# Kernel tuning notes

Hardware: AMD Instinct MI355X
Metric: run time of the kernel (lower is better)

Reference implementation:

```python
import jax, jax.numpy as jnp
import numpy as np

B = 65536   # batch (agent-timesteps)
NN = 16     # neighbors per agent
NO = 32     # obstacles per agent
SD = 4      # state_dim_per_agent
D_ROBOT = 0.3
D_OBST = 0.5
B_GAMMA = 0.01
B_EXPH = 1.0
A_MIN, A_MAX = -2.0, 2.0
PHI_MIN, PHI_MAX = -2.0, 2.0


def _mlp2(h, W1, b1, W2, b2):
    # DeepSet sub-network: activation between layers, linear last (matches
    # 'for layer in layers[:-1]: x = act(layer(x)); x = layers[-1](x)')
    return jax.nn.relu(h @ W1 + b1) @ W2 + b2


def setup_inputs() -> dict:
    key = jax.random.key(0)
    ks = jax.random.split(key, 24)
    own = jax.random.normal(ks[0], (B, SD), dtype=jnp.float32)
    # relative positions with |component| in [0.5, 2.0] so norms exceed D_* (barrier well-defined)
    npos = jax.random.uniform(ks[1], (B, NN, 2), minval=0.5, maxval=2.0) * jnp.sign(jax.random.normal(ks[2], (B, NN, 2)))
    nvel = 0.1 * jax.random.normal(ks[3], (B, NN, 2))
    neigh = jnp.concatenate([npos, nvel], axis=-1).reshape(B, 4 * NN)
    opos = (jax.random.uniform(ks[4], (B, NO, 2), minval=0.5, maxval=2.0) * jnp.sign(jax.random.normal(ks[5], (B, NO, 2)))).reshape(B, 2 * NO)
    x = jnp.concatenate([jnp.full((B, 1), float(NN), dtype=jnp.float32), own, neigh, opos], axis=1)
    noise = 0.05 * jax.random.normal(ks[6], (B, 2), dtype=jnp.float32)  # the 0.05*N(0,1) action noise, made deterministic

    def lin(k, i, o):
        return 0.1 * jax.random.normal(k, (i, o), dtype=jnp.float32)

    return {
        'x': x, 'noise': noise,
        # neighbor DeepSet: phi 4->64->16, rho 16->64->8
        'pnW1': lin(ks[7], 4, 64),  'pnb1': jnp.zeros((64,), jnp.float32),
        'pnW2': lin(ks[8], 64, 16), 'pnb2': jnp.zeros((16,), jnp.float32),
        'rnW1': lin(ks[9], 16, 64), 'rnb1': jnp.zeros((64,), jnp.float32),
        'rnW2': lin(ks[10], 64, 8), 'rnb2': jnp.zeros((8,), jnp.float32),
        # obstacle DeepSet: phi 2->64->16, rho 16->64->8
        'poW1': lin(ks[11], 2, 64),  'pob1': jnp.zeros((64,), jnp.float32),
        'poW2': lin(ks[12], 64, 16), 'pob2': jnp.zeros((16,), jnp.float32),
        'roW1': lin(ks[13], 16, 64), 'rob1': jnp.zeros((64,), jnp.float32),
        'roW2': lin(ks[14], 64, 8),  'rob2': jnp.zeros((8,), jnp.float32),
        # psi: 18 -> 64 -> 64 -> 2
        'psW1': lin(ks[15], 18, 64), 'psb1': jnp.zeros((64,), jnp.float32),
        'psW2': lin(ks[16], 64, 64), 'psb2': jnp.zeros((64,), jnp.float32),
        'psW3': lin(ks[17], 64, 2),  'psb3': jnp.zeros((2,), jnp.float32),
    }


def reference(x, noise,
              pnW1, pnb1, pnW2, pnb2, rnW1, rnb1, rnW2, rnb2,
              poW1, pob1, poW2, pob2, roW1, rob1, roW2, rob2,
              psW1, psb1, psW2, psb2, psW3, psb3):
    b = x.shape[0]
    neigh = x[:, 5:5 + 4 * NN].reshape(b, NN, 4)   # per-neighbor relative state
    obst = x[:, 5 + 4 * NN:].reshape(b, NO, 2)      # per-obstacle relative pos

    # 'empty' (learned) action: DeepSets + psi MLP
    rho_n = _mlp2(_mlp2(neigh, pnW1, pnb1, pnW2, pnb2).sum(axis=1), rnW1, rnb1, rnW2, rnb2)
    rho_o = _mlp2(_mlp2(obst, poW1, pob1, poW2, pob2).sum(axis=1), roW1, rob1, roW2, rob2)
    g = x[:, 1:3]
    h = jnp.concatenate([rho_n, rho_o, g], axis=1)
    h = jax.nn.relu(h @ psW1 + psb1)
    h = jax.nn.relu(h @ psW2 + psb2)
    h = jnp.tanh(h @ psW3 + psb3)
    empty = (h + 1.0) / 2.0 * (PHI_MAX - PHI_MIN) + PHI_MIN

    # barrier terms, vectorized over all neighbors/obstacles at once:
    # A = b_gamma * P * ||P||^-1 * (||P|| - D)^(-b_exph), summed over edges
    def barrier_sum(P, D):
        nrm = jnp.linalg.norm(P, axis=-1, keepdims=True)   # [b, E, 1]
        H = nrm - D
        return (B_GAMMA * P / (nrm * H ** B_EXPH)).sum(axis=1)

    bar = barrier_sum(-neigh[..., :2], D_ROBOT) + barrier_sum(-obst, D_OBST)

    a = jnp.tanh(empty + bar + noise)
    return (a + 1.0) / 2.0 * (A_MAX - A_MIN) + A_MIN
```

## Files before the change

kernel.cpp:

```cpp
#include <hip/hip_runtime.h>

#define NN 16
#define NO 32
#define XCOLS 133

typedef _Float16 h8v __attribute__((ext_vector_type(8)));
typedef _Float16 h2 __attribute__((ext_vector_type(2)));
typedef float f4v __attribute__((ext_vector_type(4)));
typedef unsigned ui4 __attribute__((ext_vector_type(4)));
typedef float f2u __attribute__((ext_vector_type(2), aligned(4)));

static __device__ __forceinline__ f4v MFMA(h8v a, h8v b, f4v c) {
    return __builtin_amdgcn_mfma_f32_16x16x32_f16(a, b, c, 0, 0, 0);
}
static __device__ __forceinline__ unsigned pkbits(float a, float b) {
    return __builtin_bit_cast(unsigned, __builtin_amdgcn_cvt_pkrtz(a, b));
}
static __device__ __forceinline__ h2 u2h(unsigned v) { return __builtin_bit_cast(h2, v); }

__global__ void prep_frags(
    const float* __restrict__ pnW1, const float* __restrict__ pnW2,
    const float* __restrict__ rnW1, const float* __restrict__ rnW2,
    const float* __restrict__ poW1, const float* __restrict__ poW2,
    const float* __restrict__ roW1, const float* __restrict__ roW2,
    const float* __restrict__ psW1, const float* __restrict__ psW2,
    const float* __restrict__ psW3, unsigned* __restrict__ ws)
{
    const float* Ws[11] = {pnW1,pnW2,rnW1,rnW2,poW1,poW2,roW1,roW2,psW1,psW2,psW3};
    const int Kr[11]   = {4,64,16,64,2,64,16,64,18,64,64};
    const int Nr[11]   = {64,16,64,8,64,16,64,8,64,64,2};
    const int nkc[11]  = {1,2,1,2,1,2,1,2,1,2,2};
    const int nnt[11]  = {4,1,4,1,4,1,4,1,4,4,1};
    const int base[11] = {0,1024,1536,2560,3072,4096,4608,5632,6144,7168,9216};

    const int gid = blockIdx.x * 256 + threadIdx.x;
    int start = 0;
    #pragma unroll
    for (int a2 = 0; a2 < 11; ++a2) {
        const int n = nkc[a2] * nnt[a2] * 256;
        if (gid >= start && gid < start + n) {
            const int i = gid - start;
            const float* Wm = Ws[a2];
            const int K = Kr[a2], N = Nr[a2], nt_n = nnt[a2];
            const int d = i & 3, lane = (i >> 2) & 63, t = i >> 8;
            const int nt = t % nt_n, kc = t / nt_n;
            const int k = kc * 32 + 8 * (lane >> 4) + 2 * d;
            const int col = nt * 16 + (lane & 15);
            const float v0 = (k     < K && col < N) ? Wm[(k    ) * N + col] : 0.f;
            const float v1 = (k + 1 < K && col < N) ? Wm[(k + 1) * N + col] : 0.f;
            ws[base[a2] + i] = pkbits(v0, v1);
        }
        start += n;
    }
}

__global__ __launch_bounds__(64, 4) void barrier_net_kernel(
    const float* __restrict__ x, const float* __restrict__ noise,
    const float* __restrict__ pnb1, const float* __restrict__ pnb2,
    const float* __restrict__ rnb1, const float* __restrict__ rnb2,
    const float* __restrict__ pob1, const float* __restrict__ pob2,
    const float* __restrict__ rob1, const float* __restrict__ rob2,
    const float* __restrict__ psb1, const float* __restrict__ psb2,
    const float* __restrict__ psb3,
    const unsigned* __restrict__ wsu, float* __restrict__ out)
{
    __shared__ unsigned XS[16 * 66];
    __shared__ _Float16 W[3136];

    const int l = threadIdx.x;
    const int r = l & 15;
    const int g = l >> 4;
    const int eb = blockIdx.x * 16;

    float* barf = (float*)(W + 3072);
    const h8v* FB = (const h8v*)wsu;

    {
        const float* base = x + (size_t)eb * XCOLS;
        f2u raw[16];
        #pragma unroll
        for (int it = 0; it < 16; ++it)
            raw[it] = *(const f2u*)(base + (size_t)it * XCOLS + 5 + 2 * l);
        f2u graw = {0.f, 0.f};
        if (l < 16) graw = *(const f2u*)(base + (size_t)l * XCOLS + 1);
        #pragma unroll
        for (int it = 0; it < 16; ++it)
            XS[it * 66 + l] = pkbits(raw[it][0], raw[it][1]);
        if (l < 16) XS[l * 66 + 64] = pkbits(graw[0], graw[1]);
    }

    {
        unsigned* z = (unsigned*)(W + 2048);
        #pragma unroll
        for (int i = 0; i < 8; ++i) z[l + 64 * i] = 0u;
    }

    const int rowb = r * 66;
    const int sw8 = (r & 7) << 3;
    const int sw4 = (r & 3) << 3;

    {
        float bq0 = 0.f, bq1 = 0.f;
        #pragma unroll
        for (int jj = 0; jj < 4; ++jj) {
            const h2 v = u2h(XS[rowb + 2 * (4 * g + jj)]);
            const float v0 = (float)v[0], v1 = (float)v[1];
            const float nrm = sqrtf(v0*v0 + v1*v1);
            const float cc = 0.01f * __builtin_amdgcn_rcpf(nrm * (nrm - 0.3f));
            bq0 -= cc * v0; bq1 -= cc * v1;
        }
        #pragma unroll
        for (int jj = 0; jj < 8; ++jj) {
            const h2 v = u2h(XS[rowb + 32 + 8 * g + jj]);
            const float v0 = (float)v[0], v1 = (float)v[1];
            const float nrm = sqrtf(v0*v0 + v1*v1);
            const float cc = 0.01f * __builtin_amdgcn_rcpf(nrm * (nrm - 0.5f));
            bq0 -= cc * v0; bq1 -= cc * v1;
        }
        bq0 += __shfl_xor(bq0, 16); bq0 += __shfl_xor(bq0, 32);
        bq1 += __shfl_xor(bq1, 16); bq1 += __shfl_xor(bq1, 32);
        if (g == 0) { barf[2*r] = bq0; barf[2*r + 1] = bq1; }
    }

    {
        const h8v B0 = FB[0*64 + l], B1 = FB[1*64 + l];
        const h8v B2 = FB[2*64 + l], B3 = FB[3*64 + l];
        const f4v c0 = {pnb1[r], pnb1[r], pnb1[r], pnb1[r]};
        const f4v c1 = {pnb1[16+r], pnb1[16+r], pnb1[16+r], pnb1[16+r]};
        const f4v c2 = {pnb1[32+r], pnb1[32+r], pnb1[32+r], pnb1[32+r]};
        const f4v c3 = {pnb1[48+r], pnb1[48+r], pnb1[48+r], pnb1[48+r]};
        f4v s0 = {0,0,0,0}, s1 = {0,0,0,0}, s2 = {0,0,0,0}, s3 = {0,0,0,0};
        #pragma unroll 4
        for (int j = 0; j < NN; ++j) {
            const uint2 np = *(const uint2*)&XS[rowb + 2 * j];
            ui4 au = {np.x, np.y, 0u, 0u};
            const h8v a = __builtin_bit_cast(h8v, au);
            const f4v d0 = MFMA(a, B0, c0);
            const f4v d1 = MFMA(a, B1, c1);
            const f4v d2 = MFMA(a, B2, c2);
            const f4v d3 = MFMA(a, B3, c3);
            #pragma unroll
            for (int q = 0; q < 4; ++q) {
                s0[q] += fmaxf(d0[q], 0.f); s1[q] += fmaxf(d1[q], 0.f);
                s2[q] += fmaxf(d2[q], 0.f); s3[q] += fmaxf(d3[q], 0.f);
            }
        }
        #pragma unroll
        for (int q = 0; q < 4; ++q) {
            const int e = 4 * g + q;
            const int m = (e & 7) << 3;
            W[e*64 + (( 0 + r) ^ m)] = (_Float16)s0[q];
            W[e*64 + ((16 + r) ^ m)] = (_Float16)s1[q];
            W[e*64 + ((32 + r) ^ m)] = (_Float16)s2[q];
            W[e*64 + ((48 + r) ^ m)] = (_Float16)s3[q];
        }
    }

    {
        const h8v B0 = FB[768 + 0*64 + l], B1 = FB[768 + 1*64 + l];
        const h8v B2 = FB[768 + 2*64 + l], B3 = FB[768 + 3*64 + l];
        const f4v c0 = {pob1[r], pob1[r], pob1[r], pob1[r]};
        const f4v c1 = {pob1[16+r], pob1[16+r], pob1[16+r], pob1[16+r]};
        const f4v c2 = {pob1[32+r], pob1[32+r], pob1[32+r], pob1[32+r]};
        const f4v c3 = {pob1[48+r], pob1[48+r], pob1[48+r], pob1[48+r]};
        f4v s0 = {0,0,0,0}, s1 = {0,0,0,0}, s2 = {0,0,0,0}, s3 = {0,0,0,0};
        #pragma unroll 2
        for (int t = 0; t < 16; ++t) {
            const uint2 op = *(const uint2*)&XS[rowb + 32 + 2 * t];
            ui4 au0 = {op.x, 0u, 0u, 0u};
            ui4 au1 = {op.y, 0u, 0u, 0u};
            const h8v a0 = __builtin_bit_cast(h8v, au0);
            const h8v a1 = __builtin_bit_cast(h8v, au1);
            const f4v d0 = MFMA(a0, B0, c0); const f4v e0 = MFMA(a1, B0, c0);
            const f4v d1 = MFMA(a0, B1, c1); const f4v e1 = MFMA(a1, B1, c1);
            const f4v d2 = MFMA(a0, B2, c2); const f4v e2 = MFMA(a1, B2, c2);
            const f4v d3 = MFMA(a0, B3, c3); const f4v e3 = MFMA(a1, B3, c3);
            #pragma unroll
            for (int q = 0; q < 4; ++q) {
                s0[q] += fmaxf(d0[q], 0.f) + fmaxf(e0[q], 0.f);
                s1[q] += fmaxf(d1[q], 0.f) + fmaxf(e1[q], 0.f);
                s2[q] += fmaxf(d2[q], 0.f) + fmaxf(e2[q], 0.f);
                s3[q] += fmaxf(d3[q], 0.f) + fmaxf(e3[q], 0.f);
            }
        }
        #pragma unroll
        for (int q = 0; q < 4; ++q) {
            const int e = 4 * g + q;
            const int m = (e & 7) << 3;
            W[1024 + e*64 + (( 0 + r) ^ m)] = (_Float16)s0[q];
            W[1024 + e*64 + ((16 + r) ^ m)] = (_Float16)s1[q];
            W[1024 + e*64 + ((32 + r) ^ m)] = (_Float16)s2[q];
            W[1024 + e*64 + ((48 + r) ^ m)] = (_Float16)s3[q];
        }
    }

    {
        h8v a0 = *(const h8v*)&W[r*64 + (( 0 + 8*g) ^ sw8)];
        h8v a1 = *(const h8v*)&W[r*64 + ((32 + 8*g) ^ sw8)];
        h8v b0 = FB[256 + 0*64 + l];
        h8v b1 = FB[256 + 1*64 + l];
        const float bb = 16.f * pnb2[r];
        f4v c = {bb, bb, bb, bb};
        f4v d = MFMA(a1, b1, MFMA(a0, b0, c));
        #pragma unroll
        for (int q = 0; q < 4; ++q) {
            const int row = 4 * g + q;
            W[2048 + row*32 + (r ^ ((row&3)<<3))] = (_Float16)d[q];
        }
    }
    {
        h8v a = *(const h8v*)&W[2048 + r*32 + ((8*g) ^ sw4)];
        #pragma unroll
        for (int nt = 0; nt < 4; ++nt) {
            h8v b = FB[384 + nt*64 + l];
            const float bb = rnb1[16*nt + r];
            f4v c = {bb, bb, bb, bb};
            f4v d = MFMA(a, b, c);
            #pragma unroll
            for (int q = 0; q < 4; ++q) {
                const int row = 4 * g + q;
                W[row*64 + ((16*nt + r) ^ ((row&7)<<3))] = (_Float16)fmaxf(d[q], 0.f);
            }
        }
    }
    {
        h8v a0 = *(const h8v*)&W[r*64 + (( 0 + 8*g) ^ sw8)];
        h8v a1 = *(const h8v*)&W[r*64 + ((32 + 8*g) ^ sw8)];
        h8v b0 = FB[640 + 0*64 + l];
        h8v b1 = FB[640 + 1*64 + l];
        const float bb = (r < 8) ? rnb2[r & 7] : 0.f;
        f4v c = {bb, bb, bb, bb};
        f4v d = MFMA(a1, b1, MFMA(a0, b0, c));
        if (r < 8) {
            #pragma unroll
            for (int q = 0; q < 4; ++q) {
                const int row = 4 * g + q;
                W[2560 + row*32 + (r ^ ((row&3)<<3))] = (_Float16)d[q];
            }
        }
    }
    {
        h8v a0 = *(const h8v*)&W[1024 + r*64 + (( 0 + 8*g) ^ sw8)];
        h8v a1 = *(const h8v*)&W[1024 + r*64 + ((32 + 8*g) ^ sw8)];
        h8v b0 = FB[1024 + 0*64 + l];
        h8v b1 = FB[1024 + 1*64 + l];
        const float bb = 32.f * pob2[r];
        f4v c = {bb, bb, bb, bb};
        f4v d = MFMA(a1, b1, MFMA(a0, b0, c));
        #pragma unroll
        for (int q = 0; q < 4; ++q) {
            const int row = 4 * g + q;
            W[2048 + row*32 + (r ^ ((row&3)<<3))] = (_Float16)d[q];
        }
    }
    {
        h8v a = *(const h8v*)&W[2048 + r*32 + ((8*g) ^ sw4)];
        #pragma unroll
        for (int nt = 0; nt < 4; ++nt) {
            h8v b = FB[1152 + nt*64 + l];
            const float bb = rob1[16*nt + r];
            f4v c = {bb, bb, bb, bb};
            f4v d = MFMA(a, b, c);
            #pragma unroll
            for (int q = 0; q < 4; ++q) {
                const int row = 4 * g + q;
                W[row*64 + ((16*nt + r) ^ ((row&7)<<3))] = (_Float16)fmaxf(d[q], 0.f);
            }
        }
    }
    {
        h8v a0 = *(const h8v*)&W[r*64 + (( 0 + 8*g) ^ sw8)];
        h8v a1 = *(const h8v*)&W[r*64 + ((32 + 8*g) ^ sw8)];
        h8v b0 = FB[1408 + 0*64 + l];
        h8v b1 = FB[1408 + 1*64 + l];
        const float bb = (r < 8) ? rob2[r & 7] : 0.f;
        f4v c = {bb, bb, bb, bb};
        f4v d = MFMA(a1, b1, MFMA(a0, b0, c));
        if (r < 8) {
            #pragma unroll
            for (int q = 0; q < 4; ++q) {
                const int row = 4 * g + q;
                W[2560 + row*32 + ((8 + r) ^ ((row&3)<<3))] = (_Float16)d[q];
            }
        }
    }
    if (g == 0) {
        const h2 gv = u2h(XS[rowb + 64]);
        W[2560 + r*32 + (16 ^ sw4)] = gv[0];
        W[2560 + r*32 + (17 ^ sw4)] = gv[1];
    }
    {
        h8v a = *(const h8v*)&W[2560 + r*32 + ((8*g) ^ sw4)];
        #pragma unroll
        for (int nt = 0; nt < 4; ++nt) {
            h8v b = FB[1536 + nt*64 + l];
            const float bb = psb1[16*nt + r];
            f4v c = {bb, bb, bb, bb};
            f4v d = MFMA(a, b, c);
            #pragma unroll
            for (int q = 0; q < 4; ++q) {
                const int row = 4 * g + q;
                W[1024 + row*64 + ((16*nt + r) ^ ((row&7)<<3))] = (_Float16)fmaxf(d[q], 0.f);
            }
        }
    }
    {
        h8v a0 = *(const h8v*)&W[1024 + r*64 + (( 0 + 8*g) ^ sw8)];
        h8v a1 = *(const h8v*)&W[1024 + r*64 + ((32 + 8*g) ^ sw8)];
        #pragma unroll
        for (int nt = 0; nt < 4; ++nt) {
            h8v b0 = FB[1792 + (0*4 + nt)*64 + l];
            h8v b1 = FB[1792 + (1*4 + nt)*64 + l];
            const float bb = psb2[16*nt + r];
            f4v c = {bb, bb, bb, bb};
            f4v d = MFMA(a1, b1, MFMA(a0, b0, c));
            #pragma unroll
            for (int q = 0; q < 4; ++q) {
                const int row = 4 * g + q;
                W[row*64 + ((16*nt + r) ^ ((row&7)<<3))] = (_Float16)fmaxf(d[q], 0.f);
            }
        }
    }
    f4v dOut;
    {
        h8v a0 = *(const h8v*)&W[r*64 + (( 0 + 8*g) ^ sw8)];
        h8v a1 = *(const h8v*)&W[r*64 + ((32 + 8*g) ^ sw8)];
        h8v b0 = FB[2304 + 0*64 + l];
        h8v b1 = FB[2304 + 1*64 + l];
        const float bb = (r < 2) ? psb3[r & 1] : 0.f;
        f4v c = {bb, bb, bb, bb};
        dOut = MFMA(a1, b1, MFMA(a0, b0, c));
    }
    if (r < 2) {
        #pragma unroll
        for (int q = 0; q < 4; ++q) {
            const int e = 4 * g + q;
            const float o = dOut[q];
            const float bar = barf[e*2 + r];
            const float nz = noise[2 * (size_t)(eb + e) + r];
            const float av = tanhf(2.f * tanhf(o) + bar + nz);
            out[2 * (size_t)(eb + e) + r] = 2.f * av;
        }
    }
}

extern "C" void kernel_launch(void* const* d_in, const int* in_sizes, int n_in,
                              void* d_out, int out_size, void* d_ws, size_t ws_size,
                              hipStream_t stream) {
    const float* x    = (const float*)d_in[0];
    const float* nz   = (const float*)d_in[1];
    const float* pnW1 = (const float*)d_in[2];
    const float* pnb1 = (const float*)d_in[3];
    const float* pnW2 = (const float*)d_in[4];
    const float* pnb2 = (const float*)d_in[5];
    const float* rnW1 = (const float*)d_in[6];
    const float* rnb1 = (const float*)d_in[7];
    const float* rnW2 = (const float*)d_in[8];
    const float* rnb2 = (const float*)d_in[9];
    const float* poW1 = (const float*)d_in[10];
    const float* pob1 = (const float*)d_in[11];
    const float* poW2 = (const float*)d_in[12];
    const float* pob2 = (const float*)d_in[13];
    const float* roW1 = (const float*)d_in[14];
    const float* rob1 = (const float*)d_in[15];
    const float* roW2 = (const float*)d_in[16];
    const float* rob2 = (const float*)d_in[17];
    const float* psW1 = (const float*)d_in[18];
    const float* psb1 = (const float*)d_in[19];
    const float* psW2 = (const float*)d_in[20];
    const float* psb2 = (const float*)d_in[21];
    const float* psW3 = (const float*)d_in[22];
    const float* psb3 = (const float*)d_in[23];

    unsigned* ws = (unsigned*)d_ws;
    hipLaunchKernelGGL(prep_frags, dim3(38), dim3(256), 0, stream,
        pnW1, pnW2, rnW1, rnW2, poW1, poW2, roW1, roW2, psW1, psW2, psW3, ws);

    const int b = in_sizes[0] / XCOLS;
    hipLaunchKernelGGL(barrier_net_kernel, dim3(b / 16), dim3(64), 0, stream,
        x, nz, pnb1, pnb2, rnb1, rnb2, pob1, pob2, rob1, rob2,
        psb1, psb2, psb3, ws, (float*)d_out);
}
```

Baseline: 44.68 us.

## Process two 16-row tiles per wavefront to reuse weight fragments

Each 64-thread block now handles 32 agents as two 16-row sub-tiles, with separate LDS scratch per sub-tile. Weight fragments and biases are loaded once and applied to both sub-tiles, and the independent MFMA chains are interleaved to hide latency. The goal is to cut repeated global weight loads and per-block overhead. In exchange the grid is halved, register and LDS use per wave roughly double, and launch bounds drop to 2 waves per SIMD, which may reduce occupancy.

```diff
diff --git a/kernel.cpp b/kernel.cpp
--- a/kernel.cpp
+++ b/kernel.cpp
@@ -54,7 +54,7 @@
     }
 }
 
-__global__ __launch_bounds__(64, 4) void barrier_net_kernel(
+__global__ __launch_bounds__(64, 2) void barrier_net_kernel(
     const float* __restrict__ x, const float* __restrict__ noise,
     const float* __restrict__ pnb1, const float* __restrict__ pnb2,
     const float* __restrict__ rnb1, const float* __restrict__ rnb2,
@@ -64,42 +64,50 @@
     const float* __restrict__ psb3,
     const unsigned* __restrict__ wsu, float* __restrict__ out)
 {
-    __shared__ unsigned XS[16 * 66];
-    __shared__ _Float16 W[3136];
+    __shared__ unsigned XS[32 * 66];
+    __shared__ _Float16 W[2 * 3136];
 
     const int l = threadIdx.x;
     const int r = l & 15;
     const int g = l >> 4;
-    const int eb = blockIdx.x * 16;
-
-    float* barf = (float*)(W + 3072);
+    const int eb = blockIdx.x * 32;
+
     const h8v* FB = (const h8v*)wsu;
-
-    {
-        const float* base = x + (size_t)eb * XCOLS;
-        f2u raw[16];
-        #pragma unroll
-        for (int it = 0; it < 16; ++it)
-            raw[it] = *(const f2u*)(base + (size_t)it * XCOLS + 5 + 2 * l);
-        f2u graw = {0.f, 0.f};
-        if (l < 16) graw = *(const f2u*)(base + (size_t)l * XCOLS + 1);
-        #pragma unroll
-        for (int it = 0; it < 16; ++it)
-            XS[it * 66 + l] = pkbits(raw[it][0], raw[it][1]);
-        if (l < 16) XS[l * 66 + 64] = pkbits(graw[0], graw[1]);
-    }
-
-    {
-        unsigned* z = (unsigned*)(W + 2048);
-        #pragma unroll
-        for (int i = 0; i < 8; ++i) z[l + 64 * i] = 0u;
-    }
-
-    const int rowb = r * 66;
     const int sw8 = (r & 7) << 3;
     const int sw4 = (r & 3) << 3;
 
     {
+        const float* base = x + (size_t)eb * XCOLS;
+        #pragma unroll
+        for (int half = 0; half < 2; ++half) {
+            f2u raw[16];
+            #pragma unroll
+            for (int it = 0; it < 16; ++it)
+                raw[it] = *(const f2u*)(base + (size_t)(16 * half + it) * XCOLS + 5 + 2 * l);
+            #pragma unroll
+            for (int it = 0; it < 16; ++it)
+                XS[(16 * half + it) * 66 + l] = pkbits(raw[it][0], raw[it][1]);
+        }
+        if (l < 32) {
+            const f2u graw = *(const f2u*)(base + (size_t)l * XCOLS + 1);
+            XS[l * 66 + 64] = pkbits(graw[0], graw[1]);
+        }
+    }
+
+    {
+        #pragma unroll
+        for (int s = 0; s < 2; ++s) {
+            unsigned* z = (unsigned*)(W + s * 3136 + 2048);
+            #pragma unroll
+            for (int i = 0; i < 8; ++i) z[l + 64 * i] = 0u;
+        }
+    }
+
+    #pragma unroll
+    for (int s = 0; s < 2; ++s) {
+        _Float16* Ws_ = W + s * 3136;
+        float* barf = (float*)(Ws_ + 3072);
+        const int rowb = (16 * s + r) * 66;
         float bq0 = 0.f, bq1 = 0.f;
         #pragma unroll
         for (int jj = 0; jj < 4; ++jj) {
@@ -119,8 +127,16 @@
         }
         bq0 += __shfl_xor(bq0, 16); bq0 += __shfl_xor(bq0, 32);
         bq1 += __shfl_xor(bq1, 16); bq1 += __shfl_xor(bq1, 32);
-        if (g == 0) { barf[2*r] = bq0; barf[2*r + 1] = bq1; }
-    }
+        if (g == 0) {
+            barf[2*r] = bq0; barf[2*r + 1] = bq1;
+            const h2 gv = u2h(XS[rowb + 64]);
+            Ws_[2560 + r*32 + (16 ^ sw4)] = gv[0];
+            Ws_[2560 + r*32 + (17 ^ sw4)] = gv[1];
+        }
+    }
+
+    const int rowbA = r * 66;
+    const int rowbB = (16 + r) * 66;
 
     {
         const h8v B0 = FB[0*64 + l], B1 = FB[1*64 + l];
@@ -129,30 +145,44 @@
         const f4v c1 = {pnb1[16+r], pnb1[16+r], pnb1[16+r], pnb1[16+r]};
         const f4v c2 = {pnb1[32+r], pnb1[32+r], pnb1[32+r], pnb1[32+r]};
         const f4v c3 = {pnb1[48+r], pnb1[48+r], pnb1[48+r], pnb1[48+r]};
-        f4v s0 = {0,0,0,0}, s1 = {0,0,0,0}, s2 = {0,0,0,0}, s3 = {0,0,0,0};
+        f4v sA0 = {0,0,0,0}, sA1 = {0,0,0,0}, sA2 = {0,0,0,0}, sA3 = {0,0,0,0};
+        f4v sB0 = {0,0,0,0}, sB1 = {0,0,0,0}, sB2 = {0,0,0,0}, sB3 = {0,0,0,0};
         #pragma unroll 4
         for (int j = 0; j < NN; ++j) {
-            const uint2 np = *(const uint2*)&XS[rowb + 2 * j];
-            ui4 au = {np.x, np.y, 0u, 0u};
-            const h8v a = __builtin_bit_cast(h8v, au);
-            const f4v d0 = MFMA(a, B0, c0);
-            const f4v d1 = MFMA(a, B1, c1);
-            const f4v d2 = MFMA(a, B2, c2);
-            const f4v d3 = MFMA(a, B3, c3);
+            const uint2 npA = *(const uint2*)&XS[rowbA + 2 * j];
+            const uint2 npB = *(const uint2*)&XS[rowbB + 2 * j];
+            ui4 auA = {npA.x, npA.y, 0u, 0u};
+            ui4 auB = {npB.x, npB.y, 0u, 0u};
+            const h8v aA = __builtin_bit_cast(h8v, auA);
+            const h8v aB = __builtin_bit_cast(h8v, auB);
+            const f4v dA0 = MFMA(aA, B0, c0);
+            const f4v dA1 = MFMA(aA, B1, c1);
+            const f4v dA2 = MFMA(aA, B2, c2);
+            const f4v dA3 = MFMA(aA, B3, c3);
+            const f4v dB0 = MFMA(aB, B0, c0);
+            const f4v dB1 = MFMA(aB, B1, c1);
+            const f4v dB2 = MFMA(aB, B2, c2);
+            const f4v dB3 = MFMA(aB, B3, c3);
             #pragma unroll
             for (int q = 0; q < 4; ++q) {
-                s0[q] += fmaxf(d0[q], 0.f); s1[q] += fmaxf(d1[q], 0.f);
-                s2[q] += fmaxf(d2[q], 0.f); s3[q] += fmaxf(d3[q], 0.f);
+                sA0[q] += fmaxf(dA0[q], 0.f); sA1[q] += fmaxf(dA1[q], 0.f);
+                sA2[q] += fmaxf(dA2[q], 0.f); sA3[q] += fmaxf(dA3[q], 0.f);
+                sB0[q] += fmaxf(dB0[q], 0.f); sB1[q] += fmaxf(dB1[q], 0.f);
+                sB2[q] += fmaxf(dB2[q], 0.f); sB3[q] += fmaxf(dB3[q], 0.f);
             }
         }
         #pragma unroll
         for (int q = 0; q < 4; ++q) {
             const int e = 4 * g + q;
             const int m = (e & 7) << 3;
-            W[e*64 + (( 0 + r) ^ m)] = (_Float16)s0[q];
-            W[e*64 + ((16 + r) ^ m)] = (_Float16)s1[q];
-            W[e*64 + ((32 + r) ^ m)] = (_Float16)s2[q];
-            W[e*64 + ((48 + r) ^ m)] = (_Float16)s3[q];
+            W[e*64 + (( 0 + r) ^ m)] = (_Float16)sA0[q];
+            W[e*64 + ((16 + r) ^ m)] = (_Float16)sA1[q];
+            W[e*64 + ((32 + r) ^ m)] = (_Float16)sA2[q];
+            W[e*64 + ((48 + r) ^ m)] = (_Float16)sA3[q];
+            W[3136 + e*64 + (( 0 + r) ^ m)] = (_Float16)sB0[q];
+            W[3136 + e*64 + ((16 + r) ^ m)] = (_Float16)sB1[q];
+            W[3136 + e*64 + ((32 + r) ^ m)] = (_Float16)sB2[q];
+            W[3136 + e*64 + ((48 + r) ^ m)] = (_Float16)sB3[q];
         }
     }
 
@@ -163,183 +193,230 @@
         const f4v c1 = {pob1[16+r], pob1[16+r], pob1[16+r], pob1[16+r]};
         const f4v c2 = {pob1[32+r], pob1[32+r], pob1[32+r], pob1[32+r]};
         const f4v c3 = {pob1[48+r], pob1[48+r], pob1[48+r], pob1[48+r]};
-        f4v s0 = {0,0,0,0}, s1 = {0,0,0,0}, s2 = {0,0,0,0}, s3 = {0,0,0,0};
+        f4v sA0 = {0,0,0,0}, sA1 = {0,0,0,0}, sA2 = {0,0,0,0}, sA3 = {0,0,0,0};
+        f4v sB0 = {0,0,0,0}, sB1 = {0,0,0,0}, sB2 = {0,0,0,0}, sB3 = {0,0,0,0};
         #pragma unroll 2
         for (int t = 0; t < 16; ++t) {
-            const uint2 op = *(const uint2*)&XS[rowb + 32 + 2 * t];
-            ui4 au0 = {op.x, 0u, 0u, 0u};
-            ui4 au1 = {op.y, 0u, 0u, 0u};
-            const h8v a0 = __builtin_bit_cast(h8v, au0);
-            const h8v a1 = __builtin_bit_cast(h8v, au1);
-            const f4v d0 = MFMA(a0, B0, c0); const f4v e0 = MFMA(a1, B0, c0);
-            const f4v d1 = MFMA(a0, B1, c1); const f4v e1 = MFMA(a1, B1, c1);
-            const f4v d2 = MFMA(a0, B2, c2); const f4v e2 = MFMA(a1, B2, c2);
-            const f4v d3 = MFMA(a0, B3, c3); const f4v e3 = MFMA(a1, B3, c3);
+            const uint2 opA = *(const uint2*)&XS[rowbA + 32 + 2 * t];
+            const uint2 opB = *(const uint2*)&XS[rowbB + 32 + 2 * t];
+            ui4 aA0u = {opA.x, 0u, 0u, 0u}; ui4 aA1u = {opA.y, 0u, 0u, 0u};
+            ui4 aB0u = {opB.x, 0u, 0u, 0u}; ui4 aB1u = {opB.y, 0u, 0u, 0u};
+            const h8v aA0 = __builtin_bit_cast(h8v, aA0u);
+            const h8v aA1 = __builtin_bit_cast(h8v, aA1u);
+            const h8v aB0 = __builtin_bit_cast(h8v, aB0u);
+            const h8v aB1 = __builtin_bit_cast(h8v, aB1u);
+            const f4v dA0 = MFMA(aA0, B0, c0); const f4v eA0 = MFMA(aA1, B0, c0);
+            const f4v dA1 = MFMA(aA0, B1, c1); const f4v eA1 = MFMA(aA1, B1, c1);
+            const f4v dA2 = MFMA(aA0, B2, c2); const f4v eA2 = MFMA(aA1, B2, c2);
+            const f4v dA3 = MFMA(aA0, B3, c3); const f4v eA3 = MFMA(aA1, B3, c3);
+            const f4v dB0 = MFMA(aB0, B0, c0); const f4v eB0 = MFMA(aB1, B0, c0);
+            const f4v dB1 = MFMA(aB0, B1, c1); const f4v eB1 = MFMA(aB1, B1, c1);
+            const f4v dB2 = MFMA(aB0, B2, c2); const f4v eB2 = MFMA(aB1, B2, c2);
+            const f4v dB3 = MFMA(aB0, B3, c3); const f4v eB3 = MFMA(aB1, B3, c3);
             #pragma unroll
             for (int q = 0; q < 4; ++q) {
-                s0[q] += fmaxf(d0[q], 0.f) + fmaxf(e0[q], 0.f);
-                s1[q] += fmaxf(d1[q], 0.f) + fmaxf(e1[q], 0.f);
-                s2[q] += fmaxf(d2[q], 0.f) + fmaxf(e2[q], 0.f);
-                s3[q] += fmaxf(d3[q], 0.f) + fmaxf(e3[q], 0.f);
+                sA0[q] += fmaxf(dA0[q], 0.f) + fmaxf(eA0[q], 0.f);
+                sA1[q] += fmaxf(dA1[q], 0.f) + fmaxf(eA1[q], 0.f);
+                sA2[q] += fmaxf(dA2[q], 0.f) + fmaxf(eA2[q], 0.f);
+                sA3[q] += fmaxf(dA3[q], 0.f) + fmaxf(eA3[q], 0.f);
+                sB0[q] += fmaxf(dB0[q], 0.f) + fmaxf(eB0[q], 0.f);
+                sB1[q] += fmaxf(dB1[q], 0.f) + fmaxf(eB1[q], 0.f);
+                sB2[q] += fmaxf(dB2[q], 0.f) + fmaxf(eB2[q], 0.f);
+                sB3[q] += fmaxf(dB3[q], 0.f) + fmaxf(eB3[q], 0.f);
             }
         }
         #pragma unroll
         for (int q = 0; q < 4; ++q) {
             const int e = 4 * g + q;
             const int m = (e & 7) << 3;
-            W[1024 + e*64 + (( 0 + r) ^ m)] = (_Float16)s0[q];
-            W[1024 + e*64 + ((16 + r) ^ m)] = (_Float16)s1[q];
-            W[1024 + e*64 + ((32 + r) ^ m)] = (_Float16)s2[q];
-            W[1024 + e*64 + ((48 + r) ^ m)] = (_Float16)s3[q];
-        }
-    }
-
-    {
-        h8v a0 = *(const h8v*)&W[r*64 + (( 0 + 8*g) ^ sw8)];
-        h8v a1 = *(const h8v*)&W[r*64 + ((32 + 8*g) ^ sw8)];
+            W[1024 + e*64 + (( 0 + r) ^ m)] = (_Float16)sA0[q];
+            W[1024 + e*64 + ((16 + r) ^ m)] = (_Float16)sA1[q];
+            W[1024 + e*64 + ((32 + r) ^ m)] = (_Float16)sA2[q];
+            W[1024 + e*64 + ((48 + r) ^ m)] = (_Float16)sA3[q];
+            W[3136 + 1024 + e*64 + (( 0 + r) ^ m)] = (_Float16)sB0[q];
+            W[3136 + 1024 + e*64 + ((16 + r) ^ m)] = (_Float16)sB1[q];
+            W[3136 + 1024 + e*64 + ((32 + r) ^ m)] = (_Float16)sB2[q];
+            W[3136 + 1024 + e*64 + ((48 + r) ^ m)] = (_Float16)sB3[q];
+        }
+    }
+
+    {
         h8v b0 = FB[256 + 0*64 + l];
         h8v b1 = FB[256 + 1*64 + l];
         const float bb = 16.f * pnb2[r];
-        f4v c = {bb, bb, bb, bb};
-        f4v d = MFMA(a1, b1, MFMA(a0, b0, c));
-        #pragma unroll
-        for (int q = 0; q < 4; ++q) {
-            const int row = 4 * g + q;
-            W[2048 + row*32 + (r ^ ((row&3)<<3))] = (_Float16)d[q];
-        }
-    }
-    {
-        h8v a = *(const h8v*)&W[2048 + r*32 + ((8*g) ^ sw4)];
+        const f4v c = {bb, bb, bb, bb};
+        #pragma unroll
+        for (int s = 0; s < 2; ++s) {
+            _Float16* Ws_ = W + s * 3136;
+            h8v a0 = *(const h8v*)&Ws_[r*64 + (( 0 + 8*g) ^ sw8)];
+            h8v a1 = *(const h8v*)&Ws_[r*64 + ((32 + 8*g) ^ sw8)];
+            f4v d = MFMA(a1, b1, MFMA(a0, b0, c));
+            #pragma unroll
+            for (int q = 0; q < 4; ++q) {
+                const int row = 4 * g + q;
+                Ws_[2048 + row*32 + (r ^ ((row&3)<<3))] = (_Float16)d[q];
+            }
+        }
+    }
+    {
         #pragma unroll
         for (int nt = 0; nt < 4; ++nt) {
             h8v b = FB[384 + nt*64 + l];
             const float bb = rnb1[16*nt + r];
-            f4v c = {bb, bb, bb, bb};
-            f4v d = MFMA(a, b, c);
-            #pragma unroll
-            for (int q = 0; q < 4; ++q) {
-                const int row = 4 * g + q;
-                W[row*64 + ((16*nt + r) ^ ((row&7)<<3))] = (_Float16)fmaxf(d[q], 0.f);
-            }
-        }
-    }
-    {
-        h8v a0 = *(const h8v*)&W[r*64 + (( 0 + 8*g) ^ sw8)];
-        h8v a1 = *(const h8v*)&W[r*64 + ((32 + 8*g) ^ sw8)];
+            const f4v c = {bb, bb, bb, bb};
+            #pragma unroll
+            for (int s = 0; s < 2; ++s) {
+                _Float16* Ws_ = W + s * 3136;
+                h8v a = *(const h8v*)&Ws_[2048 + r*32 + ((8*g) ^ sw4)];
+                f4v d = MFMA(a, b, c);
+                #pragma unroll
+                for (int q = 0; q < 4; ++q) {
+                    const int row = 4 * g + q;
+                    Ws_[row*64 + ((16*nt + r) ^ ((row&7)<<3))] = (_Float16)fmaxf(d[q], 0.f);
+                }
+            }
+        }
+    }
+    {
         h8v b0 = FB[640 + 0*64 + l];
         h8v b1 = FB[640 + 1*64 + l];
         const float bb = (r < 8) ? rnb2[r & 7] : 0.f;
-        f4v c = {bb, bb, bb, bb};
-        f4v d = MFMA(a1, b1, MFMA(a0, b0, c));
-        if (r < 8) {
-            #pragma unroll
-            for (int q = 0; q < 4; ++q) {
-                const int row = 4 * g + q;
-                W[2560 + row*32 + (r ^ ((row&3)<<3))] = (_Float16)d[q];
-            }
-        }
-    }
-    {
-        h8v a0 = *(const h8v*)&W[1024 + r*64 + (( 0 + 8*g) ^ sw8)];
-        h8v a1 = *(const h8v*)&W[1024 + r*64 + ((32 + 8*g) ^ sw8)];
+        const f4v c = {bb, bb, bb, bb};
+        #pragma unroll
+        for (int s = 0; s < 2; ++s) {
+            _Float16* Ws_ = W + s * 3136;
+            h8v a0 = *(const h8v*)&Ws_[r*64 + (( 0 + 8*g) ^ sw8)];
+            h8v a1 = *(const h8v*)&Ws_[r*64 + ((32 + 8*g) ^ sw8)];
+            f4v d = MFMA(a1, b1, MFMA(a0, b0, c));
+            if (r < 8) {
+                #pragma unroll
+                for (int q = 0; q < 4; ++q) {
+                    const int row = 4 * g + q;
+                    Ws_[2560 + row*32 + (r ^ ((row&3)<<3))] = (_Float16)d[q];
+                }
+            }
+        }
+    }
+    {
         h8v b0 = FB[1024 + 0*64 + l];
         h8v b1 = FB[1024 + 1*64 + l];
         const float bb = 32.f * pob2[r];
-        f4v c = {bb, bb, bb, bb};
-        f4v d = MFMA(a1, b1, MFMA(a0, b0, c));
-        #pragma unroll
-        for (int q = 0; q < 4; ++q) {
-            const int row = 4 * g + q;
-            W[2048 + row*32 + (r ^ ((row&3)<<3))] = (_Float16)d[q];
-        }
-    }
-    {
-        h8v a = *(const h8v*)&W[2048 + r*32 + ((8*g) ^ sw4)];
+        const f4v c = {bb, bb, bb, bb};
+        #pragma unroll
+        for (int s = 0; s < 2; ++s) {
+            _Float16* Ws_ = W + s * 3136;
+            h8v a0 = *(const h8v*)&Ws_[1024 + r*64 + (( 0 + 8*g) ^ sw8)];
+            h8v a1 = *(const h8v*)&Ws_[1024 + r*64 + ((32 + 8*g) ^ sw8)];
+            f4v d = MFMA(a1, b1, MFMA(a0, b0, c));
+            #pragma unroll
+            for (int q = 0; q < 4; ++q) {
+                const int row = 4 * g + q;
+                Ws_[2048 + row*32 + (r ^ ((row&3)<<3))] = (_Float16)d[q];
+            }
+        }
+    }
+    {
         #pragma unroll
         for (int nt = 0; nt < 4; ++nt) {
             h8v b = FB[1152 + nt*64 + l];
             const float bb = rob1[16*nt + r];
-            f4v c = {bb, bb, bb, bb};
-            f4v d = MFMA(a, b, c);
-            #pragma unroll
-            for (int q = 0; q < 4; ++q) {
-                const int row = 4 * g + q;
-                W[row*64 + ((16*nt + r) ^ ((row&7)<<3))] = (_Float16)fmaxf(d[q], 0.f);
-            }
-        }
-    }
-    {
-        h8v a0 = *(const h8v*)&W[r*64 + (( 0 + 8*g) ^ sw8)];
-        h8v a1 = *(const h8v*)&W[r*64 + ((32 + 8*g) ^ sw8)];
+            const f4v c = {bb, bb, bb, bb};
+            #pragma unroll
+            for (int s = 0; s < 2; ++s) {
+                _Float16* Ws_ = W + s * 3136;
+                h8v a = *(const h8v*)&Ws_[2048 + r*32 + ((8*g) ^ sw4)];
+                f4v d = MFMA(a, b, c);
+                #pragma unroll
+                for (int q = 0; q < 4; ++q) {
+                    const int row = 4 * g + q;
+                    Ws_[row*64 + ((16*nt + r) ^ ((row&7)<<3))] = (_Float16)fmaxf(d[q], 0.f);
+                }
+            }
+        }
+    }
+    {
         h8v b0 = FB[1408 + 0*64 + l];
         h8v b1 = FB[1408 + 1*64 + l];
         const float bb = (r < 8) ? rob2[r & 7] : 0.f;
-        f4v c = {bb, bb, bb, bb};
-        f4v d = MFMA(a1, b1, MFMA(a0, b0, c));
-        if (r < 8) {
-            #pragma unroll
-            for (int q = 0; q < 4; ++q) {
-                const int row = 4 * g + q;
-                W[2560 + row*32 + ((8 + r) ^ ((row&3)<<3))] = (_Float16)d[q];
-            }
-        }
-    }
-    if (g == 0) {
-        const h2 gv = u2h(XS[rowb + 64]);
-        W[2560 + r*32 + (16 ^ sw4)] = gv[0];
-        W[2560 + r*32 + (17 ^ sw4)] = gv[1];
-    }
-    {
-        h8v a = *(const h8v*)&W[2560 + r*32 + ((8*g) ^ sw4)];
+        const f4v c = {bb, bb, bb, bb};
+        #pragma unroll
+        for (int s = 0; s < 2; ++s) {
+            _Float16* Ws_ = W + s * 3136;
+            h8v a0 = *(const h8v*)&Ws_[r*64 + (( 0 + 8*g) ^ sw8)];
+            h8v a1 = *(const h8v*)&Ws_[r*64 + ((32 + 8*g) ^ sw8)];
+            f4v d = MFMA(a1, b1, MFMA(a0, b0, c));
+            if (r < 8) {
+                #pragma unroll
+                for (int q = 0; q < 4; ++q) {
+                    const int row = 4 * g + q;
+                    Ws_[2560 + row*32 + ((8 + r) ^ ((row&3)<<3))] = (_Float16)d[q];
+                }
+            }
+        }
+    }
+    {
         #pragma unroll
         for (int nt = 0; nt < 4; ++nt) {
             h8v b = FB[1536 + nt*64 + l];
             const float bb = psb1[16*nt + r];
-            f4v c = {bb, bb, bb, bb};
-            f4v d = MFMA(a, b, c);
-            #pragma unroll
-            for (int q = 0; q < 4; ++q) {
-                const int row = 4 * g + q;
-                W[1024 + row*64 + ((16*nt + r) ^ ((row&7)<<3))] = (_Float16)fmaxf(d[q], 0.f);
-            }
-        }
-    }
-    {
-        h8v a0 = *(const h8v*)&W[1024 + r*64 + (( 0 + 8*g) ^ sw8)];
-        h8v a1 = *(const h8v*)&W[1024 + r*64 + ((32 + 8*g) ^ sw8)];
+            const f4v c = {bb, bb, bb, bb};
+            #pragma unroll
+            for (int s = 0; s < 2; ++s) {
+                _Float16* Ws_ = W + s * 3136;
+                h8v a = *(const h8v*)&Ws_[2560 + r*32 + ((8*g) ^ sw4)];
+                f4v d = MFMA(a, b, c);
+                #pragma unroll
+                for (int q = 0; q < 4; ++q) {
+                    const int row = 4 * g + q;
+                    Ws_[1024 + row*64 + ((16*nt + r) ^ ((row&7)<<3))] = (_Float16)fmaxf(d[q], 0.f);
+                }
+            }
+        }
+    }
+    {
         #pragma unroll
         for (int nt = 0; nt < 4; ++nt) {
             h8v b0 = FB[1792 + (0*4 + nt)*64 + l];
             h8v b1 = FB[1792 + (1*4 + nt)*64 + l];
             const float bb = psb2[16*nt + r];
-            f4v c = {bb, bb, bb, bb};
-            f4v d = MFMA(a1, b1, MFMA(a0, b0, c));
-            #pragma unroll
-            for (int q = 0; q < 4; ++q) {
-                const int row = 4 * g + q;
-                W[row*64 + ((16*nt + r) ^ ((row&7)<<3))] = (_Float16)fmaxf(d[q], 0.f);
-            }
-        }
-    }
-    f4v dOut;
-    {
-        h8v a0 = *(const h8v*)&W[r*64 + (( 0 + 8*g) ^ sw8)];
-        h8v a1 = *(const h8v*)&W[r*64 + ((32 + 8*g) ^ sw8)];
+            const f4v c = {bb, bb, bb, bb};
+            #pragma unroll
+            for (int s = 0; s < 2; ++s) {
+                _Float16* Ws_ = W + s * 3136;
+                h8v a0 = *(const h8v*)&Ws_[1024 + r*64 + (( 0 + 8*g) ^ sw8)];
+                h8v a1 = *(const h8v*)&Ws_[1024 + r*64 + ((32 + 8*g) ^ sw8)];
+                f4v d = MFMA(a1, b1, MFMA(a0, b0, c));
+                #pragma unroll
+                for (int q = 0; q < 4; ++q) {
+                    const int row = 4 * g + q;
+                    Ws_[row*64 + ((16*nt + r) ^ ((row&7)<<3))] = (_Float16)fmaxf(d[q], 0.f);
+                }
+            }
+        }
+    }
+    {
         h8v b0 = FB[2304 + 0*64 + l];
         h8v b1 = FB[2304 + 1*64 + l];
         const float bb = (r < 2) ? psb3[r & 1] : 0.f;
-        f4v c = {bb, bb, bb, bb};
-        dOut = MFMA(a1, b1, MFMA(a0, b0, c));
-    }
-    if (r < 2) {
-        #pragma unroll
-        for (int q = 0; q < 4; ++q) {
-            const int e = 4 * g + q;
-            const float o = dOut[q];
-            const float bar = barf[e*2 + r];
-            const float nz = noise[2 * (size_t)(eb + e) + r];
-            const float av = tanhf(2.f * tanhf(o) + bar + nz);
-            out[2 * (size_t)(eb + e) + r] = 2.f * av;
+        const f4v c = {bb, bb, bb, bb};
+        #pragma unroll
+        for (int s = 0; s < 2; ++s) {
+            _Float16* Ws_ = W + s * 3136;
+            const float* barf = (const float*)(Ws_ + 3072);
+            h8v a0 = *(const h8v*)&Ws_[r*64 + (( 0 + 8*g) ^ sw8)];
+            h8v a1 = *(const h8v*)&Ws_[r*64 + ((32 + 8*g) ^ sw8)];
+            f4v dOut = MFMA(a1, b1, MFMA(a0, b0, c));
+            if (r < 2) {
+                #pragma unroll
+                for (int q = 0; q < 4; ++q) {
+                    const int e = 4 * g + q;
+                    const float o = dOut[q];
+                    const float bar = barf[e*2 + r];
+                    const float nz = noise[2 * (size_t)(eb + 16*s + e) + r];
+                    const float av = tanhf(2.f * tanhf(o) + bar + nz);
+                    out[2 * (size_t)(eb + 16*s + e) + r] = 2.f * av;
+                }
+            }
         }
     }
 }
@@ -377,7 +454,7 @@
         pnW1, pnW2, rnW1, rnW2, poW1, poW2, roW1, roW2, psW1, psW2, psW3, ws);
 
     const int b = in_sizes[0] / XCOLS;
-    hipLaunchKernelGGL(barrier_net_kernel, dim3(b / 16), dim3(64), 0, stream,
+    hipLaunchKernelGGL(barrier_net_kernel, dim3(b / 32), dim3(64), 0, stream,
         x, nz, pnb1, pnb2, rnb1, rnb2, pob1, pob2, rob1, rob2,
         psb1, psb2, psb3, ws, (float*)d_out);
 }
```

Result: slower. 58.93 us (+31.9%).
